# Kernel optimization log

Measured on AMD Instinct MI355X. Metric: run time of the kernel, lower is better.

## Reference

```python
import jax, jax.numpy as jnp
import numpy as np

NUM_HEADS = 8
LN_EPS = 1e-5


def setup_inputs() -> dict:
    key = jax.random.key(0)
    ks = jax.random.split(key, 8)
    B, H, W, C = 2, 64, 64, 256
    return {
        "x": jax.random.normal(ks[0], (B, H, W, C), dtype=jnp.float32),
        "cond": jax.random.normal(ks[1], (B, C), dtype=jnp.float32),
        "t": jax.random.randint(ks[2], (B,), 0, 100, dtype=jnp.int64),
        "emb_table": jax.random.normal(ks[3], (100, C), dtype=jnp.float32) * 0.02,
        "ada_w": jax.random.normal(ks[4], (C, 2 * C), dtype=jnp.float32) * 0.02,
        "ada_b": jnp.zeros((2 * C,), dtype=jnp.float32),
        "qkv_w": jax.random.normal(ks[5], (C, 3 * C), dtype=jnp.float32) * 0.02,
        "qkv_b": jnp.zeros((3 * C,), dtype=jnp.float32),
        "proj_w": jax.random.normal(ks[6], (C, C), dtype=jnp.float32) * 0.02,
        "proj_b": jnp.zeros((C,), dtype=jnp.float32),
    }


def reference(x, cond, t, emb_table, ada_w, ada_b, qkv_w, qkv_b, proj_w, proj_b):
    B, H, W, C = x.shape
    N = H * W
    h = NUM_HEADS
    d = C // h
    scale = d ** -0.5

    x = x.reshape(B, N, C)

    # AdaLayerNorm (adalayernorm_abs): timestep embedding -> SiLU -> Linear -> scale/shift
    emb = emb_table[t]                                # [B, C]
    ss = jax.nn.silu(emb) @ ada_w + ada_b             # [B, 2C]
    sc, sh = jnp.split(ss, 2, axis=-1)                # each [B, C]
    mu = jnp.mean(x, axis=-1, keepdims=True)
    var = jnp.var(x, axis=-1, keepdims=True)
    xn = (x - mu) * jax.lax.rsqrt(var + LN_EPS)       # LN without affine
    x = xn * (1.0 + sc[:, None, :]) + sh[:, None, :]

    # QKV projection and head split
    qkv = (x @ qkv_w + qkv_b).reshape(B, N, 3, h, d)
    qkv = jnp.transpose(qkv, (2, 0, 3, 1, 4))          # [3, B, h, N, d]
    q, k, v = qkv[0], qkv[1], qkv[2]

    # Manual attention: full [B, h, N, N] scores (matches original module)
    attn = jnp.einsum('bhnd,bhmd->bhnm', q, k) * scale
    attn = jax.nn.softmax(attn, axis=-1)
    out = jnp.einsum('bhnm,bhmd->bhnd', attn, v)       # [B, h, N, d]
    out = jnp.transpose(out, (0, 2, 1, 3)).reshape(B, N, C)

    out = (out.reshape(B, H, W, C) @ proj_w) + proj_b
    return out
```

## Files before the change

### kernel.cpp

```cpp
#include <hip/hip_runtime.h>
#include <hip/hip_bf16.h>
#include <stdint.h>

typedef __attribute__((ext_vector_type(8))) short bfrag;
typedef __attribute__((ext_vector_type(4))) short bfrag4;
typedef __attribute__((ext_vector_type(4))) float f32x4;
typedef __attribute__((ext_vector_type(2))) float f32x2;
typedef __attribute__((ext_vector_type(2))) unsigned int u32x2;
typedef __attribute__((ext_vector_type(4))) unsigned int u32x4;

__device__ inline short f2bf(float f) {
  union { float f; uint32_t u; } v; v.f = f;
  uint32_t u = v.u;
  uint32_t r = (u + 0x7fffu + ((u >> 16) & 1u)) >> 16;
  return (short)r;
}
__device__ inline float bf2f(short s) {
  return __builtin_bit_cast(float, (uint32_t)((uint32_t)(uint16_t)s << 16));
}

#if __has_builtin(__builtin_amdgcn_cvt_pk_bf16_f32)
typedef __attribute__((ext_vector_type(2))) __bf16 bf16x2_t;
__device__ inline uint32_t pack_bf16(float a, float b) {
  bf16x2_t r = __builtin_amdgcn_cvt_pk_bf16_f32(a, b);
  return __builtin_bit_cast(uint32_t, r);
}
#else
__device__ inline uint32_t pack_bf16(float a, float b) {
  uint32_t ua = __builtin_bit_cast(uint32_t, a) + 0x8000u;
  uint32_t ub = __builtin_bit_cast(uint32_t, b) + 0x8000u;
  return __builtin_amdgcn_perm(ub, ua, 0x07060302);
}
#endif

__device__ inline void lds_barrier() {
  asm volatile("s_waitcnt lgkmcnt(0)" ::: "memory");
  __builtin_amdgcn_s_barrier();
  asm volatile("" ::: "memory");
}

__global__ __launch_bounds__(256) void prep_kernel(
    const float* __restrict__ emb_table, const int* __restrict__ t,
    const float* __restrict__ ada_w, const float* __restrict__ ada_b,
    float* __restrict__ scsh,
    const float* __restrict__ qkv_w, short* __restrict__ qkv_wt,
    const float* __restrict__ proj_w, short* __restrict__ proj_wt) {
  __shared__ float smem[64 * 65];
  const int blk = blockIdx.x;
  const int tid = threadIdx.x;
  if (blk < 16) {
    float* se = smem;
    float* part = smem + 256;
    int b = blk >> 3, ox = blk & 7;
    int tt = t[b];
    float e = emb_table[tt * 256 + tid];
    se[tid] = e / (1.f + __expf(-e));
    __syncthreads();
    int ol = tid & 63, kc = tid >> 6;
    int o = ox * 64 + ol;
    float acc = 0.f;
#pragma unroll 8
    for (int k = kc * 64; k < (kc + 1) * 64; ++k) acc += se[k] * ada_w[k * 512 + o];
    part[tid] = acc;
    __syncthreads();
    if (tid < 64) {
      int oo = ox * 64 + tid;
      scsh[b * 512 + oo] =
          part[tid] + part[64 + tid] + part[128 + tid] + part[192 + tid] + ada_b[oo];
    }
  } else {
    const float* W; short* Wt; int N, lb;
    if (blk < 64) { W = qkv_w; Wt = qkv_wt; N = 768; lb = blk - 16; }
    else          { W = proj_w; Wt = proj_wt; N = 256; lb = blk - 64; }
    float (*tile)[65] = (float(*)[65])smem;
    int k0 = (lb & 3) * 64, n0 = (lb >> 2) * 64;
    int r = tid >> 2, c0 = (tid & 3) * 16;
    const float* src = W + (long)(k0 + r) * N + n0 + c0;
#pragma unroll
    for (int j = 0; j < 16; j += 4) {
      float4 v = *(const float4*)(src + j);
      tile[r][c0 + j] = v.x; tile[r][c0 + j + 1] = v.y;
      tile[r][c0 + j + 2] = v.z; tile[r][c0 + j + 3] = v.w;
    }
    __syncthreads();
    int nl = tid >> 2, kc = (tid & 3) * 16;
    short outv[16];
#pragma unroll
    for (int j = 0; j < 16; ++j) outv[j] = f2bf(tile[kc + j][nl]);
    short* dst = Wt + (long)(n0 + nl) * 256 + k0 + kc;
    *(bfrag*)dst = *(bfrag*)&outv[0];
    *(bfrag*)(dst + 8) = *(bfrag*)&outv[8];
  }
}

__global__ __launch_bounds__(256) void ln_kernel(const float* __restrict__ x,
                                                 const float* __restrict__ scsh,
                                                 short* __restrict__ xb) {
  int row = blockIdx.x * 4 + (threadIdx.x >> 6);
  int b = row >> 12;
  int lane = threadIdx.x & 63;
  float4 v = *(const float4*)(x + (long)row * 256 + lane * 4);
  float s = v.x + v.y + v.z + v.w;
  float sq = v.x * v.x + v.y * v.y + v.z * v.z + v.w * v.w;
#pragma unroll
  for (int off = 32; off > 0; off >>= 1) {
    s += __shfl_xor(s, off);
    sq += __shfl_xor(sq, off);
  }
  float mu = s * (1.f / 256.f);
  float var = sq * (1.f / 256.f) - mu * mu;
  float rstd = rsqrtf(var + 1e-5f);
  const float* scp = scsh + b * 512 + lane * 4;
  float4 sc = *(const float4*)scp;
  float4 sh = *(const float4*)(scp + 256);
  float y0 = (v.x - mu) * rstd * (1.f + sc.x) + sh.x;
  float y1 = (v.y - mu) * rstd * (1.f + sc.y) + sh.y;
  float y2 = (v.z - mu) * rstd * (1.f + sc.z) + sh.z;
  float y3 = (v.w - mu) * rstd * (1.f + sc.w) + sh.w;
  u32x2 o; o.x = pack_bf16(y0, y1); o.y = pack_bf16(y2, y3);
  *(u32x2*)&xb[(long)row * 256 + lane * 4] = o;
}

__global__ __launch_bounds__(256) void gemm_qkv(const short* __restrict__ A,
                                                const short* __restrict__ Bt,
                                                const float* __restrict__ bias,
                                                float qscale,
                                                short* __restrict__ qk,
                                                short* __restrict__ vT) {
  __shared__ short As[128 * 40];
  __shared__ short Bs[64 * 40];
  const int mt = blockIdx.x, nt = blockIdx.y;
  const int tid = threadIdx.x;
  const int w = tid >> 6, lane = tid & 63, l16 = lane & 15, quad = lane >> 4;
  const int ar = tid >> 1, ak = (tid & 1) * 16;
  const int br = tid >> 2, bk = (tid & 3) * 8;
  f32x4 acc[2][4] = {};
  const short* Arow = A + (long)(mt * 128 + ar) * 256 + ak;
  const short* Brow = Bt + (long)(nt * 64 + br) * 256 + bk;
  bfrag a8a = *(const bfrag*)Arow;
  bfrag a8b = *(const bfrag*)(Arow + 8);
  bfrag b8  = *(const bfrag*)Brow;
  for (int kk = 0; kk < 8; ++kk) {
    __syncthreads();
    *(bfrag*)&As[ar * 40 + ak] = a8a;
    *(bfrag*)&As[ar * 40 + ak + 8] = a8b;
    *(bfrag*)&Bs[br * 40 + bk] = b8;
    __syncthreads();
    int kn = (kk < 7) ? (kk + 1) : 7;
    a8a = *(const bfrag*)(Arow + kn * 32);
    a8b = *(const bfrag*)(Arow + kn * 32 + 8);
    b8  = *(const bfrag*)(Brow + kn * 32);
    bfrag a0 = *(const bfrag*)&As[(w * 32 + l16) * 40 + quad * 8];
    bfrag a1 = *(const bfrag*)&As[(w * 32 + 16 + l16) * 40 + quad * 8];
#pragma unroll
    for (int c = 0; c < 4; ++c) {
      bfrag bf = *(const bfrag*)&Bs[(c * 16 + l16) * 40 + quad * 8];
      acc[0][c] = __builtin_amdgcn_mfma_f32_16x16x32_bf16(a0, bf, acc[0][c], 0, 0, 0);
      acc[1][c] = __builtin_amdgcn_mfma_f32_16x16x32_bf16(a1, bf, acc[1][c], 0, 0, 0);
    }
  }
  const int rowb = mt * 128 + w * 32 + quad * 4;
  if (nt < 8) {
#pragma unroll
    for (int rg = 0; rg < 2; ++rg) {
      int row0 = rowb + rg * 16;
#pragma unroll
      for (int c = 0; c < 4; ++c) {
        int col = nt * 64 + c * 16 + l16;
        float bv = bias[col];
        float mult = (col < 256) ? qscale : 1.0f;
#pragma unroll
        for (int r = 0; r < 4; ++r)
          qk[(long)(row0 + r) * 512 + col] = f2bf((acc[rg][c][r] + bv) * mult);
      }
    }
  } else {
    const int bb = mt >> 5;
#pragma unroll
    for (int rg = 0; rg < 2; ++rg) {
      int keyl = (rowb + rg * 16) & 4095;
#pragma unroll
      for (int c = 0; c < 4; ++c) {
        int col = nt * 64 + c * 16 + l16;
        float bv = bias[col];
        int d = col - 512;
        u32x2 dd;
        dd.x = pack_bf16(acc[rg][c][0] + bv, acc[rg][c][1] + bv);
        dd.y = pack_bf16(acc[rg][c][2] + bv, acc[rg][c][3] + bv);
        *(u32x2*)&vT[((long)(bb * 8 + (d >> 5)) * 32 + (d & 31)) * 4096 + keyl] = dd;
      }
    }
  }
}

__global__ __launch_bounds__(256) void attn_kernel(const short* __restrict__ qk,
                                                   const short* __restrict__ vT,
                                                   short* __restrict__ OpB,
                                                   float* __restrict__ lpart) {
  const int bid = blockIdx.x;
  const int c = bid & 7, j = bid >> 3;
  const int bh = c * 2 + (j >> 7);
  const int qt = j & 31;
  const int ks = (j >> 5) & 3;
  const int b = bh >> 3, hh = bh & 7;
  const int tid = threadIdx.x;
  const int w = tid >> 6, lane = tid & 63, l16 = lane & 15, quad = lane >> 4;
  const int sig0 = ((l16 >> 2) * 8) + (l16 & 3);

  __shared__ short Ks[2][64 * 36];
  __shared__ short Vt[2][32 * 68];

  const long rowbase = (long)b * 4096;
  const int qrow0 = qt * 128 + w * 32 + l16;
  bfrag qf[2];
#pragma unroll
  for (int g = 0; g < 2; ++g)
    qf[g] = *(const bfrag*)&qk[(rowbase + qrow0 + g * 16) * 512 + hh * 32 + quad * 8];

  f32x4 olo[2] = {}, ohi[2] = {};
  f32x2 lsum[2] = {};

  const int si = tid >> 2, sk = (tid & 3) * 8;
  const int vrow = tid >> 3, vcol = (tid & 7) * 8;
  const short* ksrc = qk + rowbase * 512 + 256 + hh * 32 + (long)si * 512 + sk;
  const short* vsrc = vT + ((long)bh * 32 + vrow) * 4096 + vcol;

  const int kt0 = ks * 16;
  bfrag k8 = *(const bfrag*)(ksrc + (long)kt0 * 64 * 512);
  bfrag v8 = *(const bfrag*)(vsrc + kt0 * 64);

  int buf = 0;
  for (int i = 0; i < 16; ++i) {
    *(bfrag*)&Ks[buf][si * 36 + sk] = k8;
    *(bfrag*)&Vt[buf][vrow * 68 + vcol] = v8;
    lds_barrier();
    int nn = (i < 15) ? (i + 1) : 15;
    k8 = *(const bfrag*)(ksrc + (long)(kt0 + nn) * 64 * 512);
    v8 = *(const bfrag*)(vsrc + (kt0 + nn) * 64);

#pragma unroll
    for (int p = 0; p < 2; ++p) {
      const int kb = p * 32;
      bfrag kf0 = *(const bfrag*)&Ks[buf][(kb + sig0) * 36 + quad * 8];
      bfrag kf1 = *(const bfrag*)&Ks[buf][(kb + sig0 + 4) * 36 + quad * 8];
      f32x4 z = {0, 0, 0, 0};
      f32x4 s0[2], s1[2];
      __builtin_amdgcn_s_setprio(1);
      s0[0] = __builtin_amdgcn_mfma_f32_16x16x32_bf16(kf0, qf[0], z, 0, 0, 0);
      s0[1] = __builtin_amdgcn_mfma_f32_16x16x32_bf16(kf0, qf[1], z, 0, 0, 0);
      s1[0] = __builtin_amdgcn_mfma_f32_16x16x32_bf16(kf1, qf[0], z, 0, 0, 0);
      s1[1] = __builtin_amdgcn_mfma_f32_16x16x32_bf16(kf1, qf[1], z, 0, 0, 0);
      __builtin_amdgcn_s_setprio(0);
      bfrag pb[2];
#pragma unroll
      for (int g = 0; g < 2; ++g) {
        float e0 = __builtin_amdgcn_exp2f(s0[g][0]);
        float e1 = __builtin_amdgcn_exp2f(s0[g][1]);
        float e2 = __builtin_amdgcn_exp2f(s0[g][2]);
        float e3 = __builtin_amdgcn_exp2f(s0[g][3]);
        float f0 = __builtin_amdgcn_exp2f(s1[g][0]);
        float f1 = __builtin_amdgcn_exp2f(s1[g][1]);
        float f2 = __builtin_amdgcn_exp2f(s1[g][2]);
        float f3 = __builtin_amdgcn_exp2f(s1[g][3]);
        f32x2 pa = {e0, e1}, pbv = {e2, e3}, pc = {f0, f1}, pd = {f2, f3};
        lsum[g] += pa; lsum[g] += pbv; lsum[g] += pc; lsum[g] += pd;
        u32x4 pk;
        pk.x = pack_bf16(e0, e1); pk.y = pack_bf16(e2, e3);
        pk.z = pack_bf16(f0, f1); pk.w = pack_bf16(f2, f3);
        pb[g] = __builtin_bit_cast(bfrag, pk);
      }
      bfrag vlo = *(const bfrag*)&Vt[buf][l16 * 68 + kb + quad * 8];
      bfrag vhi = *(const bfrag*)&Vt[buf][(16 + l16) * 68 + kb + quad * 8];
      __builtin_amdgcn_s_setprio(1);
#pragma unroll
      for (int g = 0; g < 2; ++g) {
        olo[g] = __builtin_amdgcn_mfma_f32_16x16x32_bf16(pb[g], vlo, olo[g], 0, 0, 0);
        ohi[g] = __builtin_amdgcn_mfma_f32_16x16x32_bf16(pb[g], vhi, ohi[g], 0, 0, 0);
      }
      __builtin_amdgcn_s_setprio(0);
    }
    buf ^= 1;
  }
  uint16_t* Ob = (uint16_t*)OpB;
  const long obase = ((long)ks * 16 + bh) * 4096;
  const int qgb = qt * 128 + w * 32;
#pragma unroll
  for (int g = 0; g < 2; ++g) {
    float ls = lsum[g].x + lsum[g].y;
    ls += __shfl_xor(ls, 16); ls += __shfl_xor(ls, 32);
    if (quad == 0)
      lpart[obase + qrow0 + g * 16] = ls;
#pragma unroll
    for (int r = 0; r < 4; ++r) {
      int q = qgb + g * 16 + quad * 4 + r;
      uint32_t pk = pack_bf16(olo[g][r], ohi[g][r]);
      Ob[(obase + q) * 32 + l16] = (uint16_t)pk;
      Ob[(obase + q) * 32 + l16 + 16] = (uint16_t)(pk >> 16);
    }
  }
}

__global__ __launch_bounds__(256) void proj_kernel(const short* __restrict__ OpB,
                                                   const float* __restrict__ lpart,
                                                   const short* __restrict__ Bt,
                                                   const float* __restrict__ bias,
                                                   float* __restrict__ out) {
  __shared__ short As[128 * 40];
  __shared__ short Bs[64 * 40];
  const int mt = blockIdx.x, nt = blockIdx.y;
  const int tid = threadIdx.x;
  const int w = tid >> 6, lane = tid & 63, l16 = lane & 15, quad = lane >> 4;
  const int ar = tid >> 1, ak = (tid & 1) * 16;
  const int br = tid >> 2, bk = (tid & 3) * 8;
  f32x4 acc[2][4] = {};

  const int row = mt * 128 + ar;
  const int q = row & 4095, bq = row >> 12;
  const short* Brow = Bt + (long)(nt * 64 + br) * 256 + bk;

  long lb0 = (long)(bq * 8) * 4096 + q;
  bfrag pa[4][2];
  f32x4 pl;
#pragma unroll
  for (int ks = 0; ks < 4; ++ks) {
    long base = (lb0 + (long)ks * 16 * 4096) * 32 + ak;
    pa[ks][0] = *(const bfrag*)&OpB[base];
    pa[ks][1] = *(const bfrag*)&OpB[base + 8];
    pl[ks] = lpart[lb0 + (long)ks * 16 * 4096];
  }
  bfrag b8 = *(const bfrag*)Brow;

  for (int kk = 0; kk < 8; ++kk) {
    float linv = 1.f / (pl[0] + pl[1] + pl[2] + pl[3]);
    short av[16];
#pragma unroll
    for (int h = 0; h < 2; ++h) {
#pragma unroll
      for (int j = 0; j < 8; j += 2) {
        float v0 = (bf2f(pa[0][h][j]) + bf2f(pa[1][h][j]) +
                    bf2f(pa[2][h][j]) + bf2f(pa[3][h][j])) * linv;
        float v1 = (bf2f(pa[0][h][j+1]) + bf2f(pa[1][h][j+1]) +
                    bf2f(pa[2][h][j+1]) + bf2f(pa[3][h][j+1])) * linv;
        *(uint32_t*)&av[h * 8 + j] = pack_bf16(v0, v1);
      }
    }
    __syncthreads();
    *(bfrag*)&As[ar * 40 + ak] = *(bfrag*)&av[0];
    *(bfrag*)&As[ar * 40 + ak + 8] = *(bfrag*)&av[8];
    *(bfrag*)&Bs[br * 40 + bk] = b8;
    __syncthreads();
    int kn = (kk < 7) ? (kk + 1) : 7;
    long lbn = (long)(bq * 8 + kn) * 4096 + q;
#pragma unroll
    for (int ks = 0; ks < 4; ++ks) {
      long base = (lbn + (long)ks * 16 * 4096) * 32 + ak;
      pa[ks][0] = *(const bfrag*)&OpB[base];
      pa[ks][1] = *(const bfrag*)&OpB[base + 8];
      pl[ks] = lpart[lbn + (long)ks * 16 * 4096];
    }
    b8 = *(const bfrag*)(Brow + kn * 32);

    bfrag a0 = *(const bfrag*)&As[(w * 32 + l16) * 40 + quad * 8];
    bfrag a1 = *(const bfrag*)&As[(w * 32 + 16 + l16) * 40 + quad * 8];
#pragma unroll
    for (int c = 0; c < 4; ++c) {
      bfrag bf = *(const bfrag*)&Bs[(c * 16 + l16) * 40 + quad * 8];
      acc[0][c] = __builtin_amdgcn_mfma_f32_16x16x32_bf16(a0, bf, acc[0][c], 0, 0, 0);
      acc[1][c] = __builtin_amdgcn_mfma_f32_16x16x32_bf16(a1, bf, acc[1][c], 0, 0, 0);
    }
  }
  const int rowb = mt * 128 + w * 32 + quad * 4;
#pragma unroll
  for (int rg = 0; rg < 2; ++rg) {
    int row0 = rowb + rg * 16;
#pragma unroll
    for (int c = 0; c < 4; ++c) {
      int col = nt * 64 + c * 16 + l16;
      float bv = bias[col];
#pragma unroll
      for (int r = 0; r < 4; ++r)
        out[(long)(row0 + r) * 256 + col] = acc[rg][c][r] + bv;
    }
  }
}

extern "C" void kernel_launch(void* const* d_in, const int* in_sizes, int n_in,
                              void* d_out, int out_size, void* d_ws, size_t ws_size,
                              hipStream_t stream) {
  const float* x      = (const float*)d_in[0];
  const int*   t      = (const int*)d_in[2];
  const float* emb    = (const float*)d_in[3];
  const float* ada_w  = (const float*)d_in[4];
  const float* ada_b  = (const float*)d_in[5];
  const float* qkv_w  = (const float*)d_in[6];
  const float* qkv_b  = (const float*)d_in[7];
  const float* proj_w = (const float*)d_in[8];
  const float* proj_b = (const float*)d_in[9];

  char* ws = (char*)d_ws;
  float* scsh     = (float*)(ws);
  short* qkv_wt   = (short*)(ws + 4096);
  short* proj_wt  = (short*)(ws + 397312);
  short* xb       = (short*)(ws + 528384);
  short* qk_out   = (short*)(ws + 4722688);
  short* vT       = (short*)(ws + 13111296);
  short* OpB      = (short*)(ws + 21499904);
  float* lpart    = (float*)(ws + 38277120);

  const float QS = 0.17677669529663687f * 1.4426950408889634f;

  prep_kernel<<<80, 256, 0, stream>>>(emb, t, ada_w, ada_b, scsh,
                                      qkv_w, qkv_wt, proj_w, proj_wt);
  ln_kernel<<<2048, 256, 0, stream>>>(x, scsh, xb);
  gemm_qkv<<<dim3(64, 12), 256, 0, stream>>>(xb, qkv_wt, qkv_b, QS, qk_out, vT);
  attn_kernel<<<2048, 256, 0, stream>>>(qk_out, vT, OpB, lpart);
  proj_kernel<<<dim3(64, 4), 256, 0, stream>>>(OpB, lpart, proj_wt, proj_b,
                                               (float*)d_out);
}
```

Baseline: 165.9 us.

## Fuse LayerNorm stats into prep kernel, apply adaLN in QKV GEMM, shrink proj tile

Removes the separate LayerNorm kernel: the prep kernel now also computes normalized rows in fp32, and the QKV GEMM applies the adaptive scale/shift and bf16 conversion while staging A into LDS. The QKV grid is remapped to a 1D swizzled order for better cache locality. The projection GEMM uses 64-row tiles to launch twice as many blocks. The trade-off is a fp32 intermediate that doubles activation traffic into the GEMM, in exchange for one fewer launch.

```diff
diff --git a/kernel.cpp b/kernel.cpp
--- a/kernel.cpp
+++ b/kernel.cpp
@@ -44,10 +44,31 @@
     const float* __restrict__ ada_w, const float* __restrict__ ada_b,
     float* __restrict__ scsh,
     const float* __restrict__ qkv_w, short* __restrict__ qkv_wt,
-    const float* __restrict__ proj_w, short* __restrict__ proj_wt) {
+    const float* __restrict__ proj_w, short* __restrict__ proj_wt,
+    const float* __restrict__ x, float* __restrict__ xn) {
   __shared__ float smem[64 * 65];
   const int blk = blockIdx.x;
   const int tid = threadIdx.x;
+  if (blk >= 80) {
+    int row = (blk - 80) * 4 + (tid >> 6);
+    int lane = tid & 63;
+    float4 v = *(const float4*)(x + (long)row * 256 + lane * 4);
+    float s = v.x + v.y + v.z + v.w;
+    float sq = v.x * v.x + v.y * v.y + v.z * v.z + v.w * v.w;
+#pragma unroll
+    for (int off = 32; off > 0; off >>= 1) {
+      s += __shfl_xor(s, off);
+      sq += __shfl_xor(sq, off);
+    }
+    float mu = s * (1.f / 256.f);
+    float var = sq * (1.f / 256.f) - mu * mu;
+    float rstd = rsqrtf(var + 1e-5f);
+    float4 o;
+    o.x = (v.x - mu) * rstd; o.y = (v.y - mu) * rstd;
+    o.z = (v.z - mu) * rstd; o.w = (v.w - mu) * rstd;
+    *(float4*)&xn[(long)row * 256 + lane * 4] = o;
+    return;
+  }
   if (blk < 16) {
     float* se = smem;
     float* part = smem + 256;
@@ -93,35 +114,8 @@
   }
 }
 
-__global__ __launch_bounds__(256) void ln_kernel(const float* __restrict__ x,
-                                                 const float* __restrict__ scsh,
-                                                 short* __restrict__ xb) {
-  int row = blockIdx.x * 4 + (threadIdx.x >> 6);
-  int b = row >> 12;
-  int lane = threadIdx.x & 63;
-  float4 v = *(const float4*)(x + (long)row * 256 + lane * 4);
-  float s = v.x + v.y + v.z + v.w;
-  float sq = v.x * v.x + v.y * v.y + v.z * v.z + v.w * v.w;
-#pragma unroll
-  for (int off = 32; off > 0; off >>= 1) {
-    s += __shfl_xor(s, off);
-    sq += __shfl_xor(sq, off);
-  }
-  float mu = s * (1.f / 256.f);
-  float var = sq * (1.f / 256.f) - mu * mu;
-  float rstd = rsqrtf(var + 1e-5f);
-  const float* scp = scsh + b * 512 + lane * 4;
-  float4 sc = *(const float4*)scp;
-  float4 sh = *(const float4*)(scp + 256);
-  float y0 = (v.x - mu) * rstd * (1.f + sc.x) + sh.x;
-  float y1 = (v.y - mu) * rstd * (1.f + sc.y) + sh.y;
-  float y2 = (v.z - mu) * rstd * (1.f + sc.z) + sh.z;
-  float y3 = (v.w - mu) * rstd * (1.f + sc.w) + sh.w;
-  u32x2 o; o.x = pack_bf16(y0, y1); o.y = pack_bf16(y2, y3);
-  *(u32x2*)&xb[(long)row * 256 + lane * 4] = o;
-}
-
-__global__ __launch_bounds__(256) void gemm_qkv(const short* __restrict__ A,
+__global__ __launch_bounds__(256) void gemm_qkv(const float* __restrict__ A,
+                                                const float* __restrict__ scsh,
                                                 const short* __restrict__ Bt,
                                                 const float* __restrict__ bias,
                                                 float qscale,
@@ -129,26 +123,54 @@
                                                 short* __restrict__ vT) {
   __shared__ short As[128 * 40];
   __shared__ short Bs[64 * 40];
-  const int mt = blockIdx.x, nt = blockIdx.y;
+  const int bid = blockIdx.x;
+  const int cx = bid & 7, jj = bid >> 3;
+  const int mt = cx * 8 + (jj & 7);
+  const int nt = jj >> 3;
   const int tid = threadIdx.x;
   const int w = tid >> 6, lane = tid & 63, l16 = lane & 15, quad = lane >> 4;
   const int ar = tid >> 1, ak = (tid & 1) * 16;
   const int br = tid >> 2, bk = (tid & 3) * 8;
   f32x4 acc[2][4] = {};
-  const short* Arow = A + (long)(mt * 128 + ar) * 256 + ak;
+  const int arow_g = mt * 128 + ar;
+  const float* scb = scsh + (arow_g >> 12) * 512;
+  const float* Arow = A + (long)arow_g * 256 + ak;
   const short* Brow = Bt + (long)(nt * 64 + br) * 256 + bk;
-  bfrag a8a = *(const bfrag*)Arow;
-  bfrag a8b = *(const bfrag*)(Arow + 8);
+  float4 xa0 = *(const float4*)(Arow);
+  float4 xa1 = *(const float4*)(Arow + 4);
+  float4 xa2 = *(const float4*)(Arow + 8);
+  float4 xa3 = *(const float4*)(Arow + 12);
   bfrag b8  = *(const bfrag*)Brow;
   for (int kk = 0; kk < 8; ++kk) {
-    __syncthreads();
-    *(bfrag*)&As[ar * 40 + ak] = a8a;
-    *(bfrag*)&As[ar * 40 + ak + 8] = a8b;
+    int cb = kk * 32 + ak;
+    float xv[16], scv[16], shv[16];
+    *(float4*)&xv[0] = xa0; *(float4*)&xv[4] = xa1;
+    *(float4*)&xv[8] = xa2; *(float4*)&xv[12] = xa3;
+    *(float4*)&scv[0]  = *(const float4*)(scb + cb);
+    *(float4*)&scv[4]  = *(const float4*)(scb + cb + 4);
+    *(float4*)&scv[8]  = *(const float4*)(scb + cb + 8);
+    *(float4*)&scv[12] = *(const float4*)(scb + cb + 12);
+    *(float4*)&shv[0]  = *(const float4*)(scb + 256 + cb);
+    *(float4*)&shv[4]  = *(const float4*)(scb + 256 + cb + 4);
+    *(float4*)&shv[8]  = *(const float4*)(scb + 256 + cb + 8);
+    *(float4*)&shv[12] = *(const float4*)(scb + 256 + cb + 12);
+    short av[16];
+#pragma unroll
+    for (int j = 0; j < 16; j += 2) {
+      float y0 = xv[j]     * (1.f + scv[j])     + shv[j];
+      float y1 = xv[j + 1] * (1.f + scv[j + 1]) + shv[j + 1];
+      *(uint32_t*)&av[j] = pack_bf16(y0, y1);
+    }
+    __syncthreads();
+    *(bfrag*)&As[ar * 40 + ak] = *(bfrag*)&av[0];
+    *(bfrag*)&As[ar * 40 + ak + 8] = *(bfrag*)&av[8];
     *(bfrag*)&Bs[br * 40 + bk] = b8;
     __syncthreads();
     int kn = (kk < 7) ? (kk + 1) : 7;
-    a8a = *(const bfrag*)(Arow + kn * 32);
-    a8b = *(const bfrag*)(Arow + kn * 32 + 8);
+    xa0 = *(const float4*)(Arow + kn * 32);
+    xa1 = *(const float4*)(Arow + kn * 32 + 4);
+    xa2 = *(const float4*)(Arow + kn * 32 + 8);
+    xa3 = *(const float4*)(Arow + kn * 32 + 12);
     b8  = *(const bfrag*)(Brow + kn * 32);
     bfrag a0 = *(const bfrag*)&As[(w * 32 + l16) * 40 + quad * 8];
     bfrag a1 = *(const bfrag*)&As[(w * 32 + 16 + l16) * 40 + quad * 8];
@@ -305,48 +327,43 @@
                                                    const short* __restrict__ Bt,
                                                    const float* __restrict__ bias,
                                                    float* __restrict__ out) {
-  __shared__ short As[128 * 40];
+  __shared__ short As[64 * 40];
   __shared__ short Bs[64 * 40];
   const int mt = blockIdx.x, nt = blockIdx.y;
   const int tid = threadIdx.x;
   const int w = tid >> 6, lane = tid & 63, l16 = lane & 15, quad = lane >> 4;
-  const int ar = tid >> 1, ak = (tid & 1) * 16;
+  const int ar = tid >> 2, ak = (tid & 3) * 8;
   const int br = tid >> 2, bk = (tid & 3) * 8;
-  f32x4 acc[2][4] = {};
-
-  const int row = mt * 128 + ar;
+  f32x4 acc[4] = {};
+
+  const int row = mt * 64 + ar;
   const int q = row & 4095, bq = row >> 12;
   const short* Brow = Bt + (long)(nt * 64 + br) * 256 + bk;
 
   long lb0 = (long)(bq * 8) * 4096 + q;
-  bfrag pa[4][2];
+  bfrag pa[4];
   f32x4 pl;
 #pragma unroll
   for (int ks = 0; ks < 4; ++ks) {
     long base = (lb0 + (long)ks * 16 * 4096) * 32 + ak;
-    pa[ks][0] = *(const bfrag*)&OpB[base];
-    pa[ks][1] = *(const bfrag*)&OpB[base + 8];
+    pa[ks] = *(const bfrag*)&OpB[base];
     pl[ks] = lpart[lb0 + (long)ks * 16 * 4096];
   }
   bfrag b8 = *(const bfrag*)Brow;
 
   for (int kk = 0; kk < 8; ++kk) {
     float linv = 1.f / (pl[0] + pl[1] + pl[2] + pl[3]);
-    short av[16];
-#pragma unroll
-    for (int h = 0; h < 2; ++h) {
-#pragma unroll
-      for (int j = 0; j < 8; j += 2) {
-        float v0 = (bf2f(pa[0][h][j]) + bf2f(pa[1][h][j]) +
-                    bf2f(pa[2][h][j]) + bf2f(pa[3][h][j])) * linv;
-        float v1 = (bf2f(pa[0][h][j+1]) + bf2f(pa[1][h][j+1]) +
-                    bf2f(pa[2][h][j+1]) + bf2f(pa[3][h][j+1])) * linv;
-        *(uint32_t*)&av[h * 8 + j] = pack_bf16(v0, v1);
-      }
+    short av[8];
+#pragma unroll
+    for (int jj2 = 0; jj2 < 8; jj2 += 2) {
+      float v0 = (bf2f(pa[0][jj2]) + bf2f(pa[1][jj2]) +
+                  bf2f(pa[2][jj2]) + bf2f(pa[3][jj2])) * linv;
+      float v1 = (bf2f(pa[0][jj2+1]) + bf2f(pa[1][jj2+1]) +
+                  bf2f(pa[2][jj2+1]) + bf2f(pa[3][jj2+1])) * linv;
+      *(uint32_t*)&av[jj2] = pack_bf16(v0, v1);
     }
     __syncthreads();
     *(bfrag*)&As[ar * 40 + ak] = *(bfrag*)&av[0];
-    *(bfrag*)&As[ar * 40 + ak + 8] = *(bfrag*)&av[8];
     *(bfrag*)&Bs[br * 40 + bk] = b8;
     __syncthreads();
     int kn = (kk < 7) ? (kk + 1) : 7;
@@ -354,33 +371,26 @@
 #pragma unroll
     for (int ks = 0; ks < 4; ++ks) {
       long base = (lbn + (long)ks * 16 * 4096) * 32 + ak;
-      pa[ks][0] = *(const bfrag*)&OpB[base];
-      pa[ks][1] = *(const bfrag*)&OpB[base + 8];
+      pa[ks] = *(const bfrag*)&OpB[base];
       pl[ks] = lpart[lbn + (long)ks * 16 * 4096];
     }
     b8 = *(const bfrag*)(Brow + kn * 32);
 
-    bfrag a0 = *(const bfrag*)&As[(w * 32 + l16) * 40 + quad * 8];
-    bfrag a1 = *(const bfrag*)&As[(w * 32 + 16 + l16) * 40 + quad * 8];
+    bfrag a0 = *(const bfrag*)&As[(w * 16 + l16) * 40 + quad * 8];
 #pragma unroll
     for (int c = 0; c < 4; ++c) {
       bfrag bf = *(const bfrag*)&Bs[(c * 16 + l16) * 40 + quad * 8];
-      acc[0][c] = __builtin_amdgcn_mfma_f32_16x16x32_bf16(a0, bf, acc[0][c], 0, 0, 0);
-      acc[1][c] = __builtin_amdgcn_mfma_f32_16x16x32_bf16(a1, bf, acc[1][c], 0, 0, 0);
-    }
-  }
-  const int rowb = mt * 128 + w * 32 + quad * 4;
-#pragma unroll
-  for (int rg = 0; rg < 2; ++rg) {
-    int row0 = rowb + rg * 16;
-#pragma unroll
-    for (int c = 0; c < 4; ++c) {
-      int col = nt * 64 + c * 16 + l16;
-      float bv = bias[col];
-#pragma unroll
-      for (int r = 0; r < 4; ++r)
-        out[(long)(row0 + r) * 256 + col] = acc[rg][c][r] + bv;
-    }
+      acc[c] = __builtin_amdgcn_mfma_f32_16x16x32_bf16(a0, bf, acc[c], 0, 0, 0);
+    }
+  }
+  const int rowb = mt * 64 + w * 16 + quad * 4;
+#pragma unroll
+  for (int c = 0; c < 4; ++c) {
+    int col = nt * 64 + c * 16 + l16;
+    float bv = bias[col];
+#pragma unroll
+    for (int r = 0; r < 4; ++r)
+      out[(long)(rowb + r) * 256 + col] = acc[c][r] + bv;
   }
 }
 
@@ -401,19 +411,18 @@
   float* scsh     = (float*)(ws);
   short* qkv_wt   = (short*)(ws + 4096);
   short* proj_wt  = (short*)(ws + 397312);
-  short* xb       = (short*)(ws + 528384);
-  short* qk_out   = (short*)(ws + 4722688);
-  short* vT       = (short*)(ws + 13111296);
+  float* xn       = (float*)(ws + 528384);
+  short* qk_out   = (short*)(ws + 8916992);
+  short* vT       = (short*)(ws + 17305600);
   short* OpB      = (short*)(ws + 21499904);
   float* lpart    = (float*)(ws + 38277120);
 
   const float QS = 0.17677669529663687f * 1.4426950408889634f;
 
-  prep_kernel<<<80, 256, 0, stream>>>(emb, t, ada_w, ada_b, scsh,
-                                      qkv_w, qkv_wt, proj_w, proj_wt);
-  ln_kernel<<<2048, 256, 0, stream>>>(x, scsh, xb);
-  gemm_qkv<<<dim3(64, 12), 256, 0, stream>>>(xb, qkv_wt, qkv_b, QS, qk_out, vT);
+  prep_kernel<<<2128, 256, 0, stream>>>(emb, t, ada_w, ada_b, scsh,
+                                        qkv_w, qkv_wt, proj_w, proj_wt, x, xn);
+  gemm_qkv<<<768, 256, 0, stream>>>(xn, scsh, qkv_wt, qkv_b, QS, qk_out, vT);
   attn_kernel<<<2048, 256, 0, stream>>>(qk_out, vT, OpB, lpart);
-  proj_kernel<<<dim3(64, 4), 256, 0, stream>>>(OpB, lpart, proj_wt, proj_b,
-                                               (float*)d_out);
-}
+  proj_kernel<<<dim3(128, 4), 256, 0, stream>>>(OpB, lpart, proj_wt, proj_b,
+                                                (float*)d_out);
+}
```

New measurement: 170.5 us. 2.8% more time.
